# Kernel tuning notes

Measured on AMD Instinct MI355X. Metric: run time of the kernel, lower is better.

## Reference

```python
import jax, jax.numpy as jnp
import numpy as np

B, T, E, S = 32, 2048, 1024, 24

def setup_inputs() -> dict:
    key = jax.random.key(0)
    ks = jax.random.split(key, 10)
    s = 0.05  # small init for numerical stability of the recurrence
    return {
        "x": jax.random.normal(ks[0], (B, T, E), jnp.float32),
        "prev_stream": jax.random.normal(ks[1], (B, S, E), jnp.float32),
        "gate_w1": jax.random.normal(ks[2], (E // 4, E), jnp.float32) * s,
        "gate_b1": jax.random.normal(ks[3], (E // 4,), jnp.float32) * s,
        "gate_w2": jax.random.normal(ks[4], (1, E // 4), jnp.float32) * s,
        "gate_b2": jax.random.normal(ks[5], (1,), jnp.float32) * s,
        "w_ih": jax.random.normal(ks[6], (3 * E, E), jnp.float32) * s,
        "w_hh": jax.random.normal(ks[7], (3 * E, E), jnp.float32) * s,
        "b_ih": jax.random.normal(ks[8], (3 * E,), jnp.float32) * s,
        "b_hh": jax.random.normal(ks[9], (3 * E,), jnp.float32) * s,
    }


def reference(x, prev_stream, gate_w1, gate_b1, gate_w2, gate_b2, w_ih, w_hh, b_ih, b_hh):
    # The sliding buffer only exposes its last row to the recurrence, so
    # carry a single hidden state h and reconstruct the buffer at the end.
    def step(h, xt):  # h, xt: [B, E]
        # gate: Linear -> exact GELU (torch default) -> Linear -> sigmoid -> [B, 1]
        g = jax.nn.sigmoid(
            jax.nn.gelu(xt @ gate_w1.T + gate_b1, approximate=False) @ gate_w2.T + gate_b2
        )
        # torch.nn.GRUCell math
        gi = xt @ w_ih.T + b_ih   # [B, 3E]
        gh = h @ w_hh.T + b_hh    # [B, 3E]
        ir, iz, inn = jnp.split(gi, 3, axis=-1)
        hr, hz, hn = jnp.split(gh, 3, axis=-1)
        r = jax.nn.sigmoid(ir + hr)
        z = jax.nn.sigmoid(iz + hz)
        n = jnp.tanh(inn + r * hn)
        new = (1.0 - z) * n + z * h
        upd = g * new + (1.0 - g) * h
        return upd, upd

    h0 = prev_stream[:, -1, :]
    _, trace = jax.lax.scan(step, h0, jnp.swapaxes(x, 0, 1))  # trace: [T, B, E]
    trace = jnp.swapaxes(trace, 0, 1)  # [B, T, E]
    stream_len = prev_stream.shape[1]
    stream = jnp.concatenate([prev_stream, trace], axis=1)[:, -stream_len:, :]
    return stream, trace
```

## Files before the change

### kernel.cpp

```cpp
#include <hip/hip_runtime.h>
#include <hip/hip_bf16.h>
#include <math.h>


typedef __attribute__((ext_vector_type(4))) float f32x4;
typedef __attribute__((ext_vector_type(2))) float f32x2;
typedef __attribute__((ext_vector_type(8))) short bf16x8;

__device__ __forceinline__ ushort f2bf(float f) {
  unsigned int x = __float_as_uint(f);
  x += 0x7fffu + ((x >> 16) & 1u);
  return (ushort)(x >> 16);
}
__device__ __forceinline__ float bf2f(ushort u) {
  return __uint_as_float(((unsigned int)u) << 16);
}
__device__ __forceinline__ float sigf(float x) {
  return 1.0f / (1.0f + __expf(-x));
}
__device__ __forceinline__ void gload_lds16(const void* g, void* l) {
  __builtin_amdgcn_global_load_lds(
      (const __attribute__((address_space(1))) unsigned int*)g,
      (__attribute__((address_space(3))) unsigned int*)l, 16, 0, 0);
}

__global__ __launch_bounds__(256) void f32_to_bf16_k(const float* __restrict__ in,
                                                     ushort* __restrict__ out, int n) {
  int i = (blockIdx.x * 256 + threadIdx.x) * 8;
  if (i >= n) return;
  float4 a = *(const float4*)(in + i);
  float4 c = *(const float4*)(in + i + 4);
  union { ushort u[8]; uint4 v; } p;
  p.u[0]=f2bf(a.x); p.u[1]=f2bf(a.y); p.u[2]=f2bf(a.z); p.u[3]=f2bf(a.w);
  p.u[4]=f2bf(c.x); p.u[5]=f2bf(c.y); p.u[6]=f2bf(c.z); p.u[7]=f2bf(c.w);
  *(uint4*)(out + i) = p.v;
}

template<int EPI>
__global__ __launch_bounds__(256) void gemm_bt(
    const ushort* __restrict__ A, const ushort* __restrict__ Bt,
    const float* __restrict__ bias, ushort* __restrict__ C,
    int M, int N, int K)
{
  __shared__ ushort lA[128 * 32];
  __shared__ ushort lB[128 * 32];
  const int tid = threadIdx.x;
  const int lane = tid & 63, wid = tid >> 6;
  const int tiles_n = N >> 7;
  const int tm = blockIdx.x / tiles_n, tn = blockIdx.x % tiles_n;
  const int wr = wid >> 1, wc = wid & 1;

  const f32x4 zero = {0.f, 0.f, 0.f, 0.f};
  f32x4 acc[4][4];
#pragma unroll
  for (int i = 0; i < 4; ++i)
#pragma unroll
    for (int n = 0; n < 4; ++n) acc[i][n] = zero;

  const ushort* gA = A + (size_t)tm * 128 * K;
  const ushort* gB = Bt + (size_t)tn * 128 * K;
  const int k0 = (lane >> 4) * 8;

  for (int kt = 0; kt < K; kt += 32) {
    __syncthreads();
#pragma unroll
    for (int i = 0; i < 2; ++i) {
      int chunk = i * 256 + tid;
      int rr = chunk >> 2, cc = chunk & 3;
      gload_lds16(gA + (size_t)rr * K + kt + cc * 8, lA + chunk * 8);
      gload_lds16(gB + (size_t)rr * K + kt + cc * 8, lB + chunk * 8);
    }
    __syncthreads();
    bf16x8 af[4], bfv[4];
#pragma unroll
    for (int i = 0; i < 4; ++i)
      af[i] = *(const bf16x8*)(lA + (wr * 64 + i * 16 + (lane & 15)) * 32 + k0);
#pragma unroll
    for (int n = 0; n < 4; ++n)
      bfv[n] = *(const bf16x8*)(lB + (wc * 64 + n * 16 + (lane & 15)) * 32 + k0);
#pragma unroll
    for (int i = 0; i < 4; ++i)
#pragma unroll
      for (int n = 0; n < 4; ++n)
        acc[i][n] = __builtin_amdgcn_mfma_f32_16x16x32_bf16(af[i], bfv[n], acc[i][n], 0, 0, 0);
  }

#pragma unroll
  for (int i = 0; i < 4; ++i) {
#pragma unroll
    for (int n = 0; n < 4; ++n) {
#pragma unroll
      for (int j = 0; j < 4; ++j) {
        int m = tm * 128 + wr * 64 + i * 16 + (lane >> 4) * 4 + j;
        int col = tn * 128 + wc * 64 + n * 16 + (lane & 15);
        float v = acc[i][n][j] + bias[col];
        if (EPI == 0) {
          int tt = m & 2047, bb = m >> 11;
          C[(size_t)(tt * 32 + bb) * 3072 + col] = f2bf(v);
        } else {
          float gl = 0.5f * v * (1.0f + erff(v * 0.70710678f));
          C[(size_t)m * 256 + col] = f2bf(gl);
        }
      }
    }
  }
}

__global__ __launch_bounds__(256) void gate_reduce(
    const ushort* __restrict__ GH1, const float* __restrict__ w2,
    const float* __restrict__ b2, float* __restrict__ G)
{
  int row = blockIdx.x * 4 + (threadIdx.x >> 6);
  int lane = threadIdx.x & 63;
  const ushort* p = GH1 + (size_t)row * 256 + lane * 4;
  ushort4 h4 = *(const ushort4*)p;
  float4 w4 = *(const float4*)(w2 + lane * 4);
  float s = bf2f(h4.x) * w4.x + bf2f(h4.y) * w4.y + bf2f(h4.z) * w4.z + bf2f(h4.w) * w4.w;
#pragma unroll
  for (int o = 32; o > 0; o >>= 1) s += __shfl_down(s, o);
  if (lane == 0) {
    G[(row & 2047) * 32 + (row >> 11)] = sigf(s + b2[0]);
  }
}

__global__ __launch_bounds__(256) void init_scan(const float* __restrict__ prev,
                                                 ushort* __restrict__ hb,
                                                 int* __restrict__ flags)
{
  int gid = blockIdx.x * 256 + threadIdx.x;
  if (gid < 32768) {
    int bb = gid >> 10, ee = gid & 1023;
    hb[gid] = f2bf(prev[((size_t)bb * 24 + 23) * 1024 + ee]);
  }
  if (gid < 2048) flags[gid] = 0;
}

__global__ __launch_bounds__(384, 2) void scan_kernel(
    const ushort* __restrict__ GI, const float* __restrict__ G,
    const float* __restrict__ w_hh, const float* __restrict__ b_hh,
    ushort* __restrict__ hb, int* __restrict__ flags,
    float* __restrict__ out)
{
  __shared__ ushort hl[16 * 1024];
  __shared__ float ghx[4 * 96];
  const int tid = threadIdx.x;
  const int wgid = blockIdx.x;
  const int Gp = wgid >> 5;
  const int c  = wgid & 31;
  const int wid = tid >> 6, lane = tid & 63;

  const int gateW = wid >> 1;
  const int ehW = (wid & 1) * 16;

  bf16x8 bfr[32];
  {
    const float* wsrc = w_hh
        + ((size_t)(gateW * 1024 + c * 32 + ehW + (lane & 15))) * 1024
        + (lane >> 4) * 8;
#pragma unroll
    for (int kk = 0; kk < 32; ++kk) {
      float4 f0 = *(const float4*)(wsrc + kk * 32);
      float4 f1 = *(const float4*)(wsrc + kk * 32 + 4);
      union { ushort u[8]; bf16x8 v; } p;
      p.u[0]=f2bf(f0.x); p.u[1]=f2bf(f0.y); p.u[2]=f2bf(f0.z); p.u[3]=f2bf(f0.w);
      p.u[4]=f2bf(f1.x); p.u[5]=f2bf(f1.y); p.u[6]=f2bf(f1.z); p.u[7]=f2bf(f1.w);
      bfr[kk] = p.v;
    }
  }

  for (int idx = tid; idx < 1536; idx += 384) {
    int r = 4 + (idx >> 7), cc = idx & 127;
    int byte = (r * 2048 + cc * 16) ^ ((r & 7) << 4);
    uint4 z = {0u, 0u, 0u, 0u};
    *(uint4*)((char*)hl + byte) = z;
  }

  const int arow = lane & 15;
  const int k0b = (lane >> 4) * 16;
  const int abase = arow * 2048, aswz = (arow & 7) << 4;
  const char* hlc = (const char*)hl;

  const int b = tid >> 4;
  const int ep = tid & 15;
  const int brow = Gp * 4 + b;
  const int e2 = c * 32 + ep * 2;
  float bhr0=0, bhr1=0, bhz0=0, bhz1=0, bhn0=0, bhn1=0;
  float h0r = 0.f, h1r = 0.f;
  unsigned int gir = 0, giz = 0, gin = 0; float gval = 0.f;
  if (tid < 64) {
    bhr0 = b_hh[e2];        bhr1 = b_hh[e2 + 1];
    bhz0 = b_hh[1024 + e2]; bhz1 = b_hh[1025 + e2];
    bhn0 = b_hh[2048 + e2]; bhn1 = b_hh[2049 + e2];
    unsigned int v = *(const unsigned int*)(hb + (size_t)brow * 1024 + e2);
    h0r = bf2f((ushort)(v & 0xffff)); h1r = bf2f((ushort)(v >> 16));
    const ushort* gp = GI + (size_t)brow * 3072 + e2;
    gir = *(const unsigned int*)(gp);
    giz = *(const unsigned int*)(gp + 1024);
    gin = *(const unsigned int*)(gp + 2048);
    gval = G[brow];
  }

  const int* fpoll = flags + Gp * 32 + (lane & 31);

  __syncthreads();

  for (int t = 0; t < 2048; ++t) {
    if (t > 0) {
      for (;;) {
        int f = __hip_atomic_load(fpoll, __ATOMIC_RELAXED, __HIP_MEMORY_SCOPE_AGENT);
        if (__ballot(f < t) == 0ULL) break;
        __builtin_amdgcn_s_sleep(1);
      }
    }

    {
      const char* hsrc = (const char*)(hb + (size_t)(t & 3) * 32768
                                          + (size_t)Gp * 4096);
      uint4 v0, v1;
      asm volatile("global_load_dwordx4 %0, %1, off sc0 sc1"
                   : "=&v"(v0) : "v"(hsrc + tid * 16) : "memory");
      if (tid < 128) {
        asm volatile("global_load_dwordx4 %0, %1, off sc0 sc1"
                     : "=&v"(v1) : "v"(hsrc + (384 + tid) * 16) : "memory");
      }
      asm volatile("s_waitcnt vmcnt(0)" ::: "memory");
      __builtin_amdgcn_sched_barrier(0);
      int r0 = tid >> 7;
      int byte0 = (r0 * 2048 + (tid & 127) * 16) ^ ((r0 & 7) << 4);
      *(uint4*)((char*)hl + byte0) = v0;
      if (tid < 128) {
        int byte1 = (3 * 2048 + (tid & 127) * 16) ^ (3 << 4);
        *(uint4*)((char*)hl + byte1) = v1;
      }
    }
    __syncthreads();

    f32x4 acc0 = {0.f,0.f,0.f,0.f}, acc1 = {0.f,0.f,0.f,0.f};
#pragma unroll
    for (int kk = 0; kk < 32; kk += 2) {
      int ka = kk * 64 + k0b;
      bf16x8 a0 = *(const bf16x8*)(hlc + abase + ((ka) ^ aswz));
      bf16x8 a1 = *(const bf16x8*)(hlc + abase + ((ka + 64) ^ aswz));
      acc0 = __builtin_amdgcn_mfma_f32_16x16x32_bf16(a0, bfr[kk],     acc0, 0, 0, 0);
      acc1 = __builtin_amdgcn_mfma_f32_16x16x32_bf16(a1, bfr[kk + 1], acc1, 0, 0, 0);
    }
    if (lane < 16) {
      f32x4 s = acc0 + acc1;
#pragma unroll
      for (int j = 0; j < 4; ++j)
        ghx[j * 96 + gateW * 32 + ehW + lane] = s[j];
    }
    __syncthreads();

    if (tid < 64) {
      float hr0v = ghx[b * 96 + ep * 2],      hr1v = ghx[b * 96 + ep * 2 + 1];
      float hz0v = ghx[b * 96 + 32 + ep * 2], hz1v = ghx[b * 96 + 33 + ep * 2];
      float hn0v = ghx[b * 96 + 64 + ep * 2], hn1v = ghx[b * 96 + 65 + ep * 2];
      float r0 = sigf(bf2f((ushort)(gir & 0xffff)) + hr0v + bhr0);
      float r1 = sigf(bf2f((ushort)(gir >> 16))    + hr1v + bhr1);
      float z0 = sigf(bf2f((ushort)(giz & 0xffff)) + hz0v + bhz0);
      float z1 = sigf(bf2f((ushort)(giz >> 16))    + hz1v + bhz1);
      float n0 = 2.f * sigf(2.f * (bf2f((ushort)(gin & 0xffff)) + r0 * (hn0v + bhn0))) - 1.f;
      float n1 = 2.f * sigf(2.f * (bf2f((ushort)(gin >> 16))    + r1 * (hn1v + bhn1))) - 1.f;
      float nw0 = (1.f - z0) * n0 + z0 * h0r;
      float nw1 = (1.f - z1) * n1 + z1 * h1r;
      float u0 = gval * nw0 + (1.f - gval) * h0r;
      float u1 = gval * nw1 + (1.f - gval) * h1r;
      h0r = u0; h1r = u1;
      unsigned int hp = (unsigned int)f2bf(u0) | ((unsigned int)f2bf(u1) << 16);
      unsigned int* haddr = (unsigned int*)hb + (size_t)((t + 1) & 3) * 16384
                            + brow * 512 + (e2 >> 1);
      asm volatile("global_store_dword %0, %1, off sc0 sc1"
                   :: "v"(haddr), "v"(hp) : "memory");
      asm volatile("s_waitcnt vmcnt(0)" ::: "memory");
      if (tid == 0) {
        int tv = t + 1;
        asm volatile("global_store_dword %0, %1, off sc0 sc1"
                     :: "v"(flags + wgid), "v"(tv) : "memory");
      }
      f32x2 uv; uv.x = u0; uv.y = u1;
      __builtin_nontemporal_store(uv,
          (f32x2*)(out + 786432 + ((size_t)brow * 2048 + t) * 1024 + e2));
      if (t >= 2024)
        __builtin_nontemporal_store(uv,
            (f32x2*)(out + ((size_t)brow * 24 + (t - 2024)) * 1024 + e2));
      int tn1 = t < 2047 ? t + 1 : 2047;
      const ushort* gp = GI + ((size_t)tn1 * 32 + brow) * 3072 + e2;
      gir = *(const unsigned int*)(gp);
      giz = *(const unsigned int*)(gp + 1024);
      gin = *(const unsigned int*)(gp + 2048);
      gval = G[tn1 * 32 + brow];
    }
    __syncthreads();
  }
}

extern "C" void kernel_launch(void* const* d_in, const int* in_sizes, int n_in,
                              void* d_out, int out_size, void* d_ws, size_t ws_size,
                              hipStream_t stream) {
  const float* x    = (const float*)d_in[0];
  const float* prev = (const float*)d_in[1];
  const float* gw1  = (const float*)d_in[2];
  const float* gb1  = (const float*)d_in[3];
  const float* gw2  = (const float*)d_in[4];
  const float* gb2  = (const float*)d_in[5];
  const float* wih  = (const float*)d_in[6];
  const float* whh  = (const float*)d_in[7];
  const float* bih  = (const float*)d_in[8];
  const float* bhh  = (const float*)d_in[9];
  float* out = (float*)d_out;

  char* ws = (char*)d_ws;
  ushort* xb    = (ushort*)(ws);
  ushort* wbih  = (ushort*)(ws + 134217728);
  ushort* wb1   = (ushort*)(ws + 140509184);
  ushort* GI    = (ushort*)(ws + 141033472);
  ushort* GH1   = (ushort*)(ws + 543686656);
  float*  Gg    = (float*) (ws + 577241088);
  ushort* hb    = (ushort*)(ws + 577503232);
  int*    flags = (int*)   (ws + 577765376);

  f32_to_bf16_k<<<32768, 256, 0, stream>>>(x, xb, 67108864);
  f32_to_bf16_k<<<1536, 256, 0, stream>>>(wih, wbih, 3145728);
  f32_to_bf16_k<<<128, 256, 0, stream>>>(gw1, wb1, 262144);
  gemm_bt<0><<<12288, 256, 0, stream>>>(xb, wbih, bih, GI, 65536, 3072, 1024);
  gemm_bt<1><<<1024, 256, 0, stream>>>(xb, wb1, gb1, GH1, 65536, 256, 1024);
  gate_reduce<<<16384, 256, 0, stream>>>(GH1, gw2, gb2, Gg);
  init_scan<<<128, 256, 0, stream>>>(prev, hb, flags);
  scan_kernel<<<256, 384, 0, stream>>>(GI, Gg, whh, bhh, hb, flags, out);
}
```

Before: 6.438 ms.

## Embed step tags with hidden-state words to replace separate flag polling

Each hidden-state value is now stored as a 64-bit word that pairs the packed bf16 pair with its timestep tag. Consumers spin on the data itself until every tag matches, which removes the separate flag array, the store wait, and the flag write-after-data round trip on the critical serial path. The buffer goes from four-deep to double-buffered with a new layout, and the __syncthreads calls become raw s_barrier calls with lgkmcnt waits. This doubles the bytes read per poll, and the correctness of double buffering relies on the tag ordering.

```diff
diff --git a/kernel.cpp b/kernel.cpp
--- a/kernel.cpp
+++ b/kernel.cpp
@@ -124,22 +124,26 @@
 }
 
 __global__ __launch_bounds__(256) void init_scan(const float* __restrict__ prev,
-                                                 ushort* __restrict__ hb,
-                                                 int* __restrict__ flags)
+                                                 ushort* __restrict__ hb)
 {
   int gid = blockIdx.x * 256 + threadIdx.x;
-  if (gid < 32768) {
-    int bb = gid >> 10, ee = gid & 1023;
-    hb[gid] = f2bf(prev[((size_t)bb * 24 + 23) * 1024 + ee]);
-  }
-  if (gid < 2048) flags[gid] = 0;
+  if (gid >= 16384) return;
+  int Gp = gid >> 11, idx = gid & 2047;
+  int b = idx >> 9, p = idx & 511;
+  int brow = Gp * 4 + b;
+  const float* src = prev + ((size_t)brow * 24 + 23) * 1024 + p * 2;
+  unsigned int data = (unsigned int)f2bf(src[0]) | ((unsigned int)f2bf(src[1]) << 16);
+  char* base = (char*)hb;
+  *(unsigned long long*)(base + (size_t)Gp * 16384 + (size_t)idx * 8) =
+      (unsigned long long)data;
+  *(unsigned long long*)(base + 131072 + (size_t)Gp * 16384 + (size_t)idx * 8) =
+      0xFFFFFFFF00000000ULL;
 }
 
 __global__ __launch_bounds__(384, 2) void scan_kernel(
     const ushort* __restrict__ GI, const float* __restrict__ G,
     const float* __restrict__ w_hh, const float* __restrict__ b_hh,
-    ushort* __restrict__ hb, int* __restrict__ flags,
-    float* __restrict__ out)
+    ushort* __restrict__ hb, float* __restrict__ out)
 {
   __shared__ ushort hl[16 * 1024];
   __shared__ float ghx[4 * 96];
@@ -148,6 +152,7 @@
   const int Gp = wgid >> 5;
   const int c  = wgid & 31;
   const int wid = tid >> 6, lane = tid & 63;
+  char* hbb = (char*)hb;
 
   const int gateW = wid >> 1;
   const int ehW = (wid & 1) * 16;
@@ -191,7 +196,8 @@
     bhr0 = b_hh[e2];        bhr1 = b_hh[e2 + 1];
     bhz0 = b_hh[1024 + e2]; bhz1 = b_hh[1025 + e2];
     bhn0 = b_hh[2048 + e2]; bhn1 = b_hh[2049 + e2];
-    unsigned int v = *(const unsigned int*)(hb + (size_t)brow * 1024 + e2);
+    unsigned int v = *(const unsigned int*)(hbb + (size_t)Gp * 16384
+                                            + (size_t)(b * 512 + c * 16 + ep) * 8);
     h0r = bf2f((ushort)(v & 0xffff)); h1r = bf2f((ushort)(v >> 16));
     const ushort* gp = GI + (size_t)brow * 3072 + e2;
     gir = *(const unsigned int*)(gp);
@@ -200,40 +206,37 @@
     gval = G[brow];
   }
 
-  const int* fpoll = flags + Gp * 32 + (lane & 31);
-
   __syncthreads();
 
   for (int t = 0; t < 2048; ++t) {
-    if (t > 0) {
+    if (tid < 256) {
+      const char* base = hbb + (size_t)(t & 1) * 131072 + (size_t)Gp * 16384
+                         + (size_t)tid * 64;
+      uint4 v0, v1, v2, v3;
+      unsigned int tg = (unsigned int)t;
       for (;;) {
-        int f = __hip_atomic_load(fpoll, __ATOMIC_RELAXED, __HIP_MEMORY_SCOPE_AGENT);
-        if (__ballot(f < t) == 0ULL) break;
+        asm volatile("global_load_dwordx4 %0, %1, off sc0 sc1"
+                     : "=&v"(v0) : "v"(base) : "memory");
+        asm volatile("global_load_dwordx4 %0, %1, off sc0 sc1"
+                     : "=&v"(v1) : "v"(base + 16) : "memory");
+        asm volatile("global_load_dwordx4 %0, %1, off sc0 sc1"
+                     : "=&v"(v2) : "v"(base + 32) : "memory");
+        asm volatile("global_load_dwordx4 %0, %1, off sc0 sc1"
+                     : "=&v"(v3) : "v"(base + 48) : "memory");
+        asm volatile("s_waitcnt vmcnt(0)" ::: "memory");
+        if (v0.y == tg && v0.w == tg && v1.y == tg && v1.w == tg &&
+            v2.y == tg && v2.w == tg && v3.y == tg && v3.w == tg) break;
         __builtin_amdgcn_s_sleep(1);
       }
-    }
-
-    {
-      const char* hsrc = (const char*)(hb + (size_t)(t & 3) * 32768
-                                          + (size_t)Gp * 4096);
-      uint4 v0, v1;
-      asm volatile("global_load_dwordx4 %0, %1, off sc0 sc1"
-                   : "=&v"(v0) : "v"(hsrc + tid * 16) : "memory");
-      if (tid < 128) {
-        asm volatile("global_load_dwordx4 %0, %1, off sc0 sc1"
-                     : "=&v"(v1) : "v"(hsrc + (384 + tid) * 16) : "memory");
-      }
-      asm volatile("s_waitcnt vmcnt(0)" ::: "memory");
       __builtin_amdgcn_sched_barrier(0);
-      int r0 = tid >> 7;
-      int byte0 = (r0 * 2048 + (tid & 127) * 16) ^ ((r0 & 7) << 4);
-      *(uint4*)((char*)hl + byte0) = v0;
-      if (tid < 128) {
-        int byte1 = (3 * 2048 + (tid & 127) * 16) ^ (3 << 4);
-        *(uint4*)((char*)hl + byte1) = v1;
-      }
-    }
-    __syncthreads();
+      int r = tid >> 6, colb = (tid & 63) * 32, swz = (r & 7) << 4;
+      uint4 da; da.x = v0.x; da.y = v0.z; da.z = v1.x; da.w = v1.z;
+      uint4 db; db.x = v2.x; db.y = v2.z; db.z = v3.x; db.w = v3.z;
+      *(uint4*)((char*)hl + ((r * 2048 + colb) ^ swz)) = da;
+      *(uint4*)((char*)hl + ((r * 2048 + colb + 16) ^ swz)) = db;
+    }
+    asm volatile("s_waitcnt lgkmcnt(0)\n\ts_barrier" ::: "memory");
+    __builtin_amdgcn_sched_barrier(0);
 
     f32x4 acc0 = {0.f,0.f,0.f,0.f}, acc1 = {0.f,0.f,0.f,0.f};
 #pragma unroll
@@ -250,7 +253,8 @@
       for (int j = 0; j < 4; ++j)
         ghx[j * 96 + gateW * 32 + ehW + lane] = s[j];
     }
-    __syncthreads();
+    asm volatile("s_waitcnt lgkmcnt(0)\n\ts_barrier" ::: "memory");
+    __builtin_amdgcn_sched_barrier(0);
 
     if (tid < 64) {
       float hr0v = ghx[b * 96 + ep * 2],      hr1v = ghx[b * 96 + ep * 2 + 1];
@@ -268,16 +272,11 @@
       float u1 = gval * nw1 + (1.f - gval) * h1r;
       h0r = u0; h1r = u1;
       unsigned int hp = (unsigned int)f2bf(u0) | ((unsigned int)f2bf(u1) << 16);
-      unsigned int* haddr = (unsigned int*)hb + (size_t)((t + 1) & 3) * 16384
-                            + brow * 512 + (e2 >> 1);
-      asm volatile("global_store_dword %0, %1, off sc0 sc1"
-                   :: "v"(haddr), "v"(hp) : "memory");
-      asm volatile("s_waitcnt vmcnt(0)" ::: "memory");
-      if (tid == 0) {
-        int tv = t + 1;
-        asm volatile("global_store_dword %0, %1, off sc0 sc1"
-                     :: "v"(flags + wgid), "v"(tv) : "memory");
-      }
+      unsigned long long wd = ((unsigned long long)(unsigned int)(t + 1) << 32) | hp;
+      char* haddr = hbb + (size_t)((t + 1) & 1) * 131072 + (size_t)Gp * 16384
+                    + (size_t)(b * 512 + c * 16 + ep) * 8;
+      asm volatile("global_store_dwordx2 %0, %1, off sc0 sc1"
+                   :: "v"(haddr), "v"(wd) : "memory");
       f32x2 uv; uv.x = u0; uv.y = u1;
       __builtin_nontemporal_store(uv,
           (f32x2*)(out + 786432 + ((size_t)brow * 2048 + t) * 1024 + e2));
@@ -291,7 +290,8 @@
       gin = *(const unsigned int*)(gp + 2048);
       gval = G[tn1 * 32 + brow];
     }
-    __syncthreads();
+    asm volatile("s_waitcnt lgkmcnt(0)\n\ts_barrier" ::: "memory");
+    __builtin_amdgcn_sched_barrier(0);
   }
 }
 
@@ -318,7 +318,6 @@
   ushort* GH1   = (ushort*)(ws + 543686656);
   float*  Gg    = (float*) (ws + 577241088);
   ushort* hb    = (ushort*)(ws + 577503232);
-  int*    flags = (int*)   (ws + 577765376);
 
   f32_to_bf16_k<<<32768, 256, 0, stream>>>(x, xb, 67108864);
   f32_to_bf16_k<<<1536, 256, 0, stream>>>(wih, wbih, 3145728);
@@ -326,6 +325,6 @@
   gemm_bt<0><<<12288, 256, 0, stream>>>(xb, wbih, bih, GI, 65536, 3072, 1024);
   gemm_bt<1><<<1024, 256, 0, stream>>>(xb, wb1, gb1, GH1, 65536, 256, 1024);
   gate_reduce<<<16384, 256, 0, stream>>>(GH1, gw2, gb2, Gg);
-  init_scan<<<128, 256, 0, stream>>>(prev, hb, flags);
-  scan_kernel<<<256, 384, 0, stream>>>(GI, Gg, whh, bhh, hb, flags, out);
-}
+  init_scan<<<64, 256, 0, stream>>>(prev, hb);
+  scan_kernel<<<256, 384, 0, stream>>>(GI, Gg, whh, bhh, hb, out);
+}
```

Measured after the change: 5.914 ms (median of 2 runs). 1.09x faster.
